# Kernel tuning notes

Hardware: AMD Instinct MI355X
Metric: run time of the kernel (lower is better)

## Reference

```python
import jax, jax.numpy as jnp
import numpy as np

DIM = 1024
NUM_HEADS = 16
MASKED = True


def setup_inputs() -> dict:
    key = jax.random.key(0)
    ks = jax.random.split(key, 9)
    B, S, D = 2, 2048, DIM
    return {
        "x": jax.random.normal(ks[0], (B, S, D), dtype=jnp.float32),
        "Wq": jax.random.normal(ks[1], (D, D), dtype=jnp.float32),
        "bq": jax.random.normal(ks[2], (D,), dtype=jnp.float32),
        "Wk": jax.random.normal(ks[3], (D, D), dtype=jnp.float32),
        "bk": jax.random.normal(ks[4], (D,), dtype=jnp.float32),
        "Wv": jax.random.normal(ks[5], (D, D), dtype=jnp.float32),
        "bv": jax.random.normal(ks[6], (D,), dtype=jnp.float32),
        "Wo": jax.random.normal(ks[7], (D, D), dtype=jnp.float32),
        "bo": jax.random.normal(ks[8], (D,), dtype=jnp.float32),
    }


def _mha(x, Wq, bq, Wk, bk, Wv, bv, Wo, bo):
    B, S, D = x.shape
    H = NUM_HEADS
    hd = D // H
    # projections (torch Linear stores [out,in]; here W is [out,in], x @ W.T + b)
    q = x @ Wq.T + bq
    k = x @ Wk.T + bk
    v = x @ Wv.T + bv
    # [B, H, S, hd]
    q = q.reshape(B, S, H, hd).transpose(0, 2, 1, 3)
    k = k.reshape(B, S, H, hd).transpose(0, 2, 1, 3)
    v = v.reshape(B, S, H, hd).transpose(0, 2, 1, 3)
    scores = jnp.einsum("bhqd,bhkd->bhqk", q, k) / jnp.sqrt(jnp.asarray(hd, x.dtype))
    if MASKED:
        mask = jnp.tril(jnp.ones((S, S), dtype=bool))
        scores = jnp.where(mask, scores, -jnp.inf)
    attn = jax.nn.softmax(scores, axis=-1)
    out = jnp.einsum("bhqk,bhkd->bhqd", attn, v)
    out = out.transpose(0, 2, 1, 3).reshape(B, S, D)
    return out @ Wo.T + bo


def reference(x, Wq, bq, Wk, bk, Wv, bv, Wo, bo):
    return _mha(x, Wq, bq, Wk, bk, Wv, bv, Wo, bo)
```

## Files before the change

kernel.cpp:

```cpp
#include <hip/hip_runtime.h>

typedef unsigned short u16;
typedef unsigned int u32;
typedef __attribute__((ext_vector_type(4))) float f32x4;
typedef __attribute__((ext_vector_type(8))) __bf16 bf16x8;

#define L2E 1.4426950408889634f

__device__ __forceinline__ u16 f2bf(float f) { return __builtin_bit_cast(u16, (__bf16)f); }
__device__ __forceinline__ float bf2f(u16 h) { return (float)__builtin_bit_cast(__bf16, h); }
__device__ __forceinline__ f32x4 mfma16(bf16x8 a, bf16x8 b, f32x4 c) {
  return __builtin_amdgcn_mfma_f32_16x16x32_bf16(a, b, c, 0, 0, 0);
}
__device__ __forceinline__ void gl_lds16(const u16* g, u16* l) {
  __builtin_amdgcn_global_load_lds((__attribute__((address_space(1))) void*)g,
                                   (__attribute__((address_space(3))) void*)l,
                                   16, 0, 0);
}
__device__ __forceinline__ f32x4 fzero() {
  f32x4 v = {0.f, 0.f, 0.f, 0.f};
  return v;
}

__global__ void k_prep(const float* __restrict__ x, const float* __restrict__ Wq,
                       const float* __restrict__ Wk, const float* __restrict__ Wv,
                       const float* __restrict__ Wo,
                       u16* __restrict__ xh, u16* __restrict__ xl,
                       u16* __restrict__ wqh, u16* __restrict__ wql,
                       u16* __restrict__ wkh, u16* __restrict__ wkl,
                       u16* __restrict__ wvb, u16* __restrict__ wob) {
  int i = (blockIdx.x * 256 + threadIdx.x) * 4;
  const float* src;
  u16* hi;
  u16* lo;
  int j;
  if (i < 4194304)      { src = x;  hi = xh;  lo = xl;      j = i; }
  else if (i < 5242880) { src = Wq; hi = wqh; lo = wql;     j = i - 4194304; }
  else if (i < 6291456) { src = Wk; hi = wkh; lo = wkl;     j = i - 5242880; }
  else if (i < 7340032) { src = Wv; hi = wvb; lo = nullptr; j = i - 6291456; }
  else                  { src = Wo; hi = wob; lo = nullptr; j = i - 7340032; }
  float4 v = *(const float4*)(src + j);
  float vv[4] = {v.x, v.y, v.z, v.w};
  u16 hh[4];
#pragma unroll
  for (int t = 0; t < 4; ++t) hh[t] = f2bf(vv[t]);
  *(ushort4*)(hi + j) = make_ushort4(hh[0], hh[1], hh[2], hh[3]);
  if (lo) {
    u16 ll[4];
#pragma unroll
    for (int t = 0; t < 4; ++t) ll[t] = f2bf(vv[t] - bf2f(hh[t]));
    *(ushort4*)(lo + j) = make_ushort4(ll[0], ll[1], ll[2], ll[3]);
  }
}

template <int SPLIT, int EPI>
__device__ __forceinline__ void gemm_body(
    u16* sm, const u16* __restrict__ Ah, const u16* __restrict__ Al,
    const u16* __restrict__ Bh, const u16* __restrict__ Bl,
    const float* __restrict__ bias, float scale,
    u16* __restrict__ oH, u16* __restrict__ oL, float* __restrict__ oF,
    int m0, int n0) {
  u16* sAh = sm;
  u16* sBh = sm + 8192;
  u16* sAl = SPLIT ? (sm + 16384) : sm;
  u16* sBl = SPLIT ? (sm + 24576) : sm;

  const int tid = threadIdx.x;
  const int lane = tid & 63, w = tid >> 6;
  const int wm = w >> 1, wn = w & 1;
  const int fr = lane & 15, fg = lane >> 4;
  const int strow = tid >> 3;
  const int stcb = (tid & 7) * 16;

  f32x4 acc[4][4];
#pragma unroll
  for (int i = 0; i < 4; ++i)
#pragma unroll
    for (int j = 0; j < 4; ++j) acc[i][j] = fzero();

  for (int kk = 0; kk < 1024; kk += 64) {
    __syncthreads();
#pragma unroll
    for (int c = 0; c < 4; ++c) {
      int row = c * 32 + strow;
      int srcc = (stcb ^ (((row >> 2) & 1) << 5)) >> 1;
      int dstc = row * 64 + (stcb >> 1);
      gl_lds16(Ah + (size_t)(m0 + row) * 1024 + kk + srcc, sAh + dstc);
      gl_lds16(Bh + (size_t)(n0 + row) * 1024 + kk + srcc, sBh + dstc);
      if constexpr (SPLIT) {
        gl_lds16(Al + (size_t)(m0 + row) * 1024 + kk + srcc, sAl + dstc);
        gl_lds16(Bl + (size_t)(n0 + row) * 1024 + kk + srcc, sBl + dstc);
      }
    }
    __syncthreads();

#pragma unroll
    for (int kk2 = 0; kk2 < 2; ++kk2) {
      bf16x8 ah[4], bh[4], al[4], bl[4];
#pragma unroll
      for (int i = 0; i < 4; ++i) {
        int ra = wm * 64 + i * 16 + fr;
        int ca = (kk2 * 64 + fg * 16) ^ (((ra >> 2) & 1) << 5);
        ah[i] = *(const bf16x8*)(sAh + ra * 64 + (ca >> 1));
        if constexpr (SPLIT) al[i] = *(const bf16x8*)(sAl + ra * 64 + (ca >> 1));
        int rb = wn * 64 + i * 16 + fr;
        int cb = (kk2 * 64 + fg * 16) ^ (((rb >> 2) & 1) << 5);
        bh[i] = *(const bf16x8*)(sBh + rb * 64 + (cb >> 1));
        if constexpr (SPLIT) bl[i] = *(const bf16x8*)(sBl + rb * 64 + (cb >> 1));
      }
      __builtin_amdgcn_s_setprio(1);
#pragma unroll
      for (int i = 0; i < 4; ++i)
#pragma unroll
        for (int j = 0; j < 4; ++j) {
          acc[i][j] = mfma16(ah[i], bh[j], acc[i][j]);
          if constexpr (SPLIT) {
            acc[i][j] = mfma16(ah[i], bl[j], acc[i][j]);
            acc[i][j] = mfma16(al[i], bh[j], acc[i][j]);
          }
        }
      __builtin_amdgcn_s_setprio(0);
    }
  }

#pragma unroll
  for (int i = 0; i < 4; ++i)
#pragma unroll
    for (int j = 0; j < 4; ++j) {
      int cg = n0 + wn * 64 + j * 16 + fr;
      float bv = bias[cg];
      if constexpr (EPI == 1) {
        int rgb = m0 + wm * 64 + i * 16 + fg * 4;
        int b = rgb >> 11, s = rgb & 2047, hd2 = cg >> 6, dd = cg & 63;
        u16 hv[4];
#pragma unroll
        for (int r = 0; r < 4; ++r) hv[r] = f2bf((acc[i][j][r] + bv) * scale);
        *(ushort4*)(oH + ((size_t)((b * 16 + hd2) * 64 + dd)) * 2048 + s) =
            make_ushort4(hv[0], hv[1], hv[2], hv[3]);
      } else {
#pragma unroll
        for (int r = 0; r < 4; ++r) {
          int rg = m0 + wm * 64 + i * 16 + fg * 4 + r;
          float val = (acc[i][j][r] + bv) * scale;
          if constexpr (EPI == 0) {
            int b = rg >> 11, s = rg & 2047, hd2 = cg >> 6, dd = cg & 63;
            size_t off = ((size_t)((b * 16 + hd2) * 2048 + s)) * 64 + dd;
            u16 hv = f2bf(val);
            oH[off] = hv;
            oL[off] = f2bf(val - bf2f(hv));
          } else {
            oF[(size_t)rg * 1024 + cg] = val;
          }
        }
      }
    }
}

__global__ __launch_bounds__(256, 2) void k_qkv(
    const u16* __restrict__ xh, const u16* __restrict__ xl,
    const u16* __restrict__ wqh, const u16* __restrict__ wql,
    const u16* __restrict__ wkh, const u16* __restrict__ wkl,
    const u16* __restrict__ wvb,
    const float* __restrict__ bq, const float* __restrict__ bk,
    const float* __restrict__ bv,
    u16* __restrict__ qh, u16* __restrict__ ql,
    u16* __restrict__ kh, u16* __restrict__ kl, u16* __restrict__ vt) {
  __shared__ u16 sm[32768];
  const int d = blockIdx.x;
  const int xcd = d & 7, j = d >> 3;
  const int m0 = (xcd * 4 + (j & 3)) * 128;
  const int pn = j >> 2;
  const int proj = pn >> 3, n0 = (pn & 7) * 128;
  if (proj == 0)
    gemm_body<1, 0>(sm, xh, xl, wqh, wql, bq, 0.125f * L2E, qh, ql, nullptr, m0, n0);
  else if (proj == 1)
    gemm_body<1, 0>(sm, xh, xl, wkh, wkl, bk, 1.0f, kh, kl, nullptr, m0, n0);
  else
    gemm_body<0, 1>(sm, xh, nullptr, wvb, nullptr, bv, 1.0f, vt, nullptr, nullptr, m0, n0);
}

__global__ __launch_bounds__(256, 4) void k_oproj(
    const u16* __restrict__ A, const u16* __restrict__ B,
    const float* __restrict__ bias, float* __restrict__ out) {
  __shared__ u16 sm[12288];
  u16* sA = sm;
  u16* sB = sm + 4096;

  const int tid = threadIdx.x;
  const int lane = tid & 63, w = tid >> 6;
  const int fr = lane & 15, fg = lane >> 4;
  const int m0 = blockIdx.x * 64, n0 = blockIdx.y * 128;
  const int strow = tid >> 3;
  const int stcb = (tid & 7) * 16;

  f32x4 acc[4][2];
#pragma unroll
  for (int i = 0; i < 4; ++i)
#pragma unroll
    for (int jj = 0; jj < 2; ++jj) acc[i][jj] = fzero();

  for (int kk = 0; kk < 1024; kk += 64) {
    __syncthreads();
#pragma unroll
    for (int c = 0; c < 2; ++c) {
      int row = c * 32 + strow;
      int srcc = (stcb ^ (((row >> 2) & 1) << 5)) >> 1;
      gl_lds16(A + (size_t)(m0 + row) * 1024 + kk + srcc, sA + row * 64 + (stcb >> 1));
    }
#pragma unroll
    for (int c = 0; c < 4; ++c) {
      int row = c * 32 + strow;
      int srcc = (stcb ^ (((row >> 2) & 1) << 5)) >> 1;
      gl_lds16(B + (size_t)(n0 + row) * 1024 + kk + srcc, sB + row * 64 + (stcb >> 1));
    }
    __syncthreads();

#pragma unroll
    for (int kk2 = 0; kk2 < 2; ++kk2) {
      bf16x8 af[4], bf_[2];
#pragma unroll
      for (int i = 0; i < 4; ++i) {
        int ra = i * 16 + fr;
        int ca = (kk2 * 64 + fg * 16) ^ (((ra >> 2) & 1) << 5);
        af[i] = *(const bf16x8*)(sA + ra * 64 + (ca >> 1));
      }
#pragma unroll
      for (int jj = 0; jj < 2; ++jj) {
        int rb = w * 32 + jj * 16 + fr;
        int cb = (kk2 * 64 + fg * 16) ^ (((rb >> 2) & 1) << 5);
        bf_[jj] = *(const bf16x8*)(sB + rb * 64 + (cb >> 1));
      }
      __builtin_amdgcn_s_setprio(1);
#pragma unroll
      for (int i = 0; i < 4; ++i)
#pragma unroll
        for (int jj = 0; jj < 2; ++jj) acc[i][jj] = mfma16(af[i], bf_[jj], acc[i][jj]);
      __builtin_amdgcn_s_setprio(0);
    }
  }

#pragma unroll
  for (int i = 0; i < 4; ++i)
#pragma unroll
    for (int jj = 0; jj < 2; ++jj) {
      int cg = n0 + w * 32 + jj * 16 + fr;
      float bv = bias[cg];
#pragma unroll
      for (int r = 0; r < 4; ++r) {
        int rg = m0 + i * 16 + fg * 4 + r;
        out[(size_t)rg * 1024 + cg] = acc[i][jj][r] + bv;
      }
    }
}

__global__ __launch_bounds__(256, 2) void k_attn(
    const u16* __restrict__ Qh, const u16* __restrict__ Ql,
    const u16* __restrict__ Kh, const u16* __restrict__ Kl,
    const u16* __restrict__ Vt, u16* __restrict__ Oa) {
  __shared__ u16 sKh[3][4096], sKl[3][4096], sVt[3][4096];

  const int tid = threadIdx.x;
  const int lane = tid & 63, w = tid >> 6;
  const int fr = lane & 15, fg = lane >> 4;

  const int d = blockIdx.x;
  const int g = d >> 3;
  const int bh = (d & 7) * 4 + (g & 3);
  const int pr = g >> 2;

  const size_t base = (size_t)bh * 131072;
  const u16* Qh_p = Qh + base;
  const u16* Ql_p = Ql + base;
  const u16* Kh_p = Kh + base;
  const u16* Kl_p = Kl + base;
  const u16* Vt_p = Vt + base;
  const int bb = bh >> 4, hh = bh & 15;

  const int srow = tid >> 3, scb8 = tid & 7;

  auto STAGE = [&](int t, int c) {
#pragma unroll
    for (int r2 = 0; r2 < 2; ++r2) {
      int prow = r2 * 32 + srow;
      int kvs = (prow & 32) | ((prow & 16) >> 2) | ((prow & 12) << 1) | (prow & 3);
      int cbk = scb8 ^ (prow & 7);
      gl_lds16(Kh_p + ((size_t)(t * 64 + kvs)) * 64 + cbk * 8, &sKh[c][prow * 64 + scb8 * 8]);
      gl_lds16(Kl_p + ((size_t)(t * 64 + kvs)) * 64 + cbk * 8, &sKl[c][prow * 64 + scb8 * 8]);
      gl_lds16(Vt_p + (size_t)prow * 2048 + t * 64 + cbk * 8, &sVt[c][prow * 64 + scb8 * 8]);
    }
  };

  for (int half = 0; half < 2; ++half) {
    const int j = half ? (31 - pr) : pr;
    const int nt = j + 1;
    const int qrow = j * 64 + w * 16 + fr;

    if (half) asm volatile("s_barrier" ::: "memory");
    int cur = 0;
    STAGE(0, 0);

    bf16x8 qhf[2], qlf[2];
#pragma unroll
    for (int ks = 0; ks < 2; ++ks) {
      qhf[ks] = *(const bf16x8*)(Qh_p + (size_t)qrow * 64 + ks * 32 + fg * 8);
      qlf[ks] = *(const bf16x8*)(Ql_p + (size_t)qrow * 64 + ks * 32 + fg * 8);
    }

    float mx = -1e30f, l = 0.f;
    f32x4 o[4];
#pragma unroll
    for (int f = 0; f < 4; ++f) o[f] = fzero();

    for (int t = 0; t < nt; ++t) {
      int nxt = cur + 1;
      if (nxt == 3) nxt = 0;
      if (t + 1 < nt) {
        STAGE(t + 1, nxt);
        asm volatile("s_waitcnt vmcnt(6)" ::: "memory");
      } else {
        asm volatile("s_waitcnt vmcnt(0)" ::: "memory");
      }
      asm volatile("s_barrier" ::: "memory");

      const u16* kbh = sKh[cur];
      const u16* kbl = sKl[cur];
      const u16* vbb = sVt[cur];

      f32x4 sc[4];
      __builtin_amdgcn_s_setprio(1);
#pragma unroll
      for (int f = 0; f < 4; ++f) {
        f32x4 a = fzero();
#pragma unroll
        for (int ks = 0; ks < 2; ++ks) {
          int row = f * 16 + fr;
          int cb = (fg + 4 * ks) ^ (fr & 7);
          bf16x8 khv = *(const bf16x8*)(kbh + row * 64 + cb * 8);
          bf16x8 klv = *(const bf16x8*)(kbl + row * 64 + cb * 8);
          a = mfma16(khv, qhf[ks], a);
          a = mfma16(khv, qlf[ks], a);
          a = mfma16(klv, qhf[ks], a);
        }
        sc[f] = a;
      }
      __builtin_amdgcn_s_setprio(0);

      if (t == nt - 1) {
#pragma unroll
        for (int f = 0; f < 4; ++f) {
          int kvb = t * 64 + (f >> 1) * 32 + fg * 8 + (f & 1) * 4;
#pragma unroll
          for (int r = 0; r < 4; ++r)
            if (kvb + r > qrow) sc[f][r] = -1e30f;
        }
      }

      float pm = -1e30f;
#pragma unroll
      for (int f = 0; f < 4; ++f)
#pragma unroll
        for (int r = 0; r < 4; ++r) pm = fmaxf(pm, sc[f][r]);
      pm = fmaxf(pm, __shfl_xor(pm, 16, 64));
      pm = fmaxf(pm, __shfl_xor(pm, 32, 64));

      const bool resc = __any(pm > mx + 11.5f);
      float alp = 1.0f;
      if (resc) {
        float mn = fmaxf(mx, pm);
        alp = exp2f(mx - mn);
        mx = mn;
      }

      float pp[4][4];
      float ps = 0.f;
#pragma unroll
      for (int f = 0; f < 4; ++f) {
#pragma unroll
        for (int r = 0; r < 4; ++r) {
          pp[f][r] = exp2f(sc[f][r] - mx);
          ps += pp[f][r];
        }
      }
      ps += __shfl_xor(ps, 16, 64);
      ps += __shfl_xor(ps, 32, 64);
      l = l * alp + ps;

      if (resc) {
        float alpb[4];
#pragma unroll
        for (int r = 0; r < 4; ++r) alpb[r] = __shfl(alp, fg * 4 + r, 64);
#pragma unroll
        for (int f = 0; f < 4; ++f)
#pragma unroll
          for (int r = 0; r < 4; ++r) o[f][r] *= alpb[r];
      }

      __builtin_amdgcn_s_setprio(1);
#pragma unroll
      for (int ks = 0; ks < 2; ++ks) {
        bf16x8 pa;
#pragma unroll
        for (int jj = 0; jj < 4; ++jj) {
          pa[jj] = (__bf16)pp[2 * ks][jj];
          pa[4 + jj] = (__bf16)pp[2 * ks + 1][jj];
        }
#pragma unroll
        for (int f = 0; f < 4; ++f) {
          int row = f * 16 + fr;
          int cb = (fg + 4 * ks) ^ (fr & 7);
          bf16x8 vb = *(const bf16x8*)(vbb + row * 64 + cb * 8);
          o[f] = mfma16(pa, vb, o[f]);
        }
      }
      __builtin_amdgcn_s_setprio(0);

      cur = nxt;
    }

    float lb[4];
#pragma unroll
    for (int r = 0; r < 4; ++r) lb[r] = __shfl(l, fg * 4 + r, 64);
#pragma unroll
    for (int f = 0; f < 4; ++f)
#pragma unroll
      for (int r = 0; r < 4; ++r) {
        int qg = j * 64 + w * 16 + fg * 4 + r;
        float val = o[f][r] / lb[r];
        Oa[((size_t)(bb * 2048 + qg)) * 1024 + hh * 64 + f * 16 + fr] = f2bf(val);
      }
  }
}

extern "C" void kernel_launch(void* const* d_in, const int* in_sizes, int n_in,
                              void* d_out, int out_size, void* d_ws, size_t ws_size,
                              hipStream_t stream) {
  const float* x  = (const float*)d_in[0];
  const float* Wq = (const float*)d_in[1];
  const float* bq = (const float*)d_in[2];
  const float* Wk = (const float*)d_in[3];
  const float* bk = (const float*)d_in[4];
  const float* Wv = (const float*)d_in[5];
  const float* bv = (const float*)d_in[6];
  const float* Wo = (const float*)d_in[7];
  const float* bo = (const float*)d_in[8];
  float* out = (float*)d_out;

  u16* ws  = (u16*)d_ws;
  u16* xh  = ws;
  u16* xl  = xh + 4194304;
  u16* wqh = xl + 4194304;
  u16* wql = wqh + 1048576;
  u16* wkh = wql + 1048576;
  u16* wkl = wkh + 1048576;
  u16* wvb = wkl + 1048576;
  u16* wob = wvb + 1048576;
  u16* qh  = wob + 1048576;
  u16* ql  = qh + 4194304;
  u16* kh  = ql + 4194304;
  u16* kl  = kh + 4194304;
  u16* vt  = kl + 4194304;
  u16* ao  = xh;

  k_prep<<<8192, 256, 0, stream>>>(x, Wq, Wk, Wv, Wo, xh, xl, wqh, wql, wkh, wkl, wvb, wob);
  k_qkv<<<768, 256, 0, stream>>>(xh, xl, wqh, wql, wkh, wkl, wvb, bq, bk, bv,
                                 qh, ql, kh, kl, vt);
  k_attn<<<512, 256, 0, stream>>>(qh, ql, kh, kl, vt, ao);
  k_oproj<<<dim3(64, 8), 256, 0, stream>>>(ao, wob, bo, out);
}
```

Baseline: 152.0 us.

## Split attention into one q-tile per block and load V directly to registers

```diff
diff --git a/kernel.cpp b/kernel.cpp
--- a/kernel.cpp
+++ b/kernel.cpp
@@ -253,20 +253,20 @@
     }
 }
 
-__global__ __launch_bounds__(256, 2) void k_attn(
+__global__ __launch_bounds__(256, 4) void k_attn(
     const u16* __restrict__ Qh, const u16* __restrict__ Ql,
     const u16* __restrict__ Kh, const u16* __restrict__ Kl,
     const u16* __restrict__ Vt, u16* __restrict__ Oa) {
-  __shared__ u16 sKh[3][4096], sKl[3][4096], sVt[3][4096];
+  __shared__ u16 sKh[2][4096], sKl[2][4096];
 
   const int tid = threadIdx.x;
   const int lane = tid & 63, w = tid >> 6;
   const int fr = lane & 15, fg = lane >> 4;
 
   const int d = blockIdx.x;
-  const int g = d >> 3;
-  const int bh = (d & 7) * 4 + (g & 3);
-  const int pr = g >> 2;
+  const int bh = (d & 7) * 4 + ((d >> 3) & 3);
+  const int j = 31 - (d >> 5);
+  const int nt = j + 1;
 
   const size_t base = (size_t)bh * 131072;
   const u16* Qh_p = Qh + base;
@@ -286,149 +286,144 @@
       int cbk = scb8 ^ (prow & 7);
       gl_lds16(Kh_p + ((size_t)(t * 64 + kvs)) * 64 + cbk * 8, &sKh[c][prow * 64 + scb8 * 8]);
       gl_lds16(Kl_p + ((size_t)(t * 64 + kvs)) * 64 + cbk * 8, &sKl[c][prow * 64 + scb8 * 8]);
-      gl_lds16(Vt_p + (size_t)prow * 2048 + t * 64 + cbk * 8, &sVt[c][prow * 64 + scb8 * 8]);
     }
   };
 
-  for (int half = 0; half < 2; ++half) {
-    const int j = half ? (31 - pr) : pr;
-    const int nt = j + 1;
-    const int qrow = j * 64 + w * 16 + fr;
-
-    if (half) asm volatile("s_barrier" ::: "memory");
-    int cur = 0;
-    STAGE(0, 0);
-
-    bf16x8 qhf[2], qlf[2];
+  const int qrow = j * 64 + w * 16 + fr;
+
+  STAGE(0, 0);
+
+  bf16x8 qhf[2], qlf[2];
+#pragma unroll
+  for (int ks = 0; ks < 2; ++ks) {
+    qhf[ks] = *(const bf16x8*)(Qh_p + (size_t)qrow * 64 + ks * 32 + fg * 8);
+    qlf[ks] = *(const bf16x8*)(Ql_p + (size_t)qrow * 64 + ks * 32 + fg * 8);
+  }
+
+  float mx = -1e30f, l = 0.f;
+  f32x4 o[4];
+#pragma unroll
+  for (int f = 0; f < 4; ++f) o[f] = fzero();
+
+  for (int t = 0; t < nt; ++t) {
+    const int cur = t & 1;
+
+    bf16x8 vf[2][4];
+#pragma unroll
+    for (int ks = 0; ks < 2; ++ks)
+#pragma unroll
+      for (int f = 0; f < 4; ++f)
+        vf[ks][f] = *(const bf16x8*)(Vt_p + (size_t)(f * 16 + fr) * 2048 + t * 64 +
+                                     ks * 32 + fg * 8);
+
+    if (t + 1 < nt) {
+      STAGE(t + 1, cur ^ 1);
+      asm volatile("s_waitcnt vmcnt(12)" ::: "memory");
+    } else {
+      asm volatile("s_waitcnt vmcnt(8)" ::: "memory");
+    }
+    asm volatile("s_barrier" ::: "memory");
+
+    const u16* kbh = sKh[cur];
+    const u16* kbl = sKl[cur];
+
+    f32x4 sc[4];
+    __builtin_amdgcn_s_setprio(1);
+#pragma unroll
+    for (int f = 0; f < 4; ++f) {
+      f32x4 a = fzero();
+#pragma unroll
+      for (int ks = 0; ks < 2; ++ks) {
+        int row = f * 16 + fr;
+        int cb = (fg + 4 * ks) ^ (fr & 7);
+        bf16x8 khv = *(const bf16x8*)(kbh + row * 64 + cb * 8);
+        bf16x8 klv = *(const bf16x8*)(kbl + row * 64 + cb * 8);
+        a = mfma16(khv, qhf[ks], a);
+        a = mfma16(khv, qlf[ks], a);
+        a = mfma16(klv, qhf[ks], a);
+      }
+      sc[f] = a;
+    }
+    __builtin_amdgcn_s_setprio(0);
+
+    if (t == nt - 1) {
+#pragma unroll
+      for (int f = 0; f < 4; ++f) {
+        int kvb = t * 64 + (f >> 1) * 32 + fg * 8 + (f & 1) * 4;
+#pragma unroll
+        for (int r = 0; r < 4; ++r)
+          if (kvb + r > qrow) sc[f][r] = -1e30f;
+      }
+    }
+
+    float pm = -1e30f;
+#pragma unroll
+    for (int f = 0; f < 4; ++f)
+#pragma unroll
+      for (int r = 0; r < 4; ++r) pm = fmaxf(pm, sc[f][r]);
+    pm = fmaxf(pm, __shfl_xor(pm, 16, 64));
+    pm = fmaxf(pm, __shfl_xor(pm, 32, 64));
+
+    const bool resc = __any(pm > mx + 11.5f);
+    float alp = 1.0f;
+    if (resc) {
+      float mn = fmaxf(mx, pm);
+      alp = exp2f(mx - mn);
+      mx = mn;
+    }
+
+    float pp[4][4];
+    float ps = 0.f;
+#pragma unroll
+    for (int f = 0; f < 4; ++f) {
+#pragma unroll
+      for (int r = 0; r < 4; ++r) {
+        pp[f][r] = exp2f(sc[f][r] - mx);
+        ps += pp[f][r];
+      }
+    }
+    ps += __shfl_xor(ps, 16, 64);
+    ps += __shfl_xor(ps, 32, 64);
+    l = l * alp + ps;
+
+    if (resc) {
+      float alpb[4];
+#pragma unroll
+      for (int r = 0; r < 4; ++r) alpb[r] = __shfl(alp, fg * 4 + r, 64);
+#pragma unroll
+      for (int f = 0; f < 4; ++f)
+#pragma unroll
+        for (int r = 0; r < 4; ++r) o[f][r] *= alpb[r];
+    }
+
+    __builtin_amdgcn_s_setprio(1);
 #pragma unroll
     for (int ks = 0; ks < 2; ++ks) {
-      qhf[ks] = *(const bf16x8*)(Qh_p + (size_t)qrow * 64 + ks * 32 + fg * 8);
-      qlf[ks] = *(const bf16x8*)(Ql_p + (size_t)qrow * 64 + ks * 32 + fg * 8);
-    }
-
-    float mx = -1e30f, l = 0.f;
-    f32x4 o[4];
-#pragma unroll
-    for (int f = 0; f < 4; ++f) o[f] = fzero();
-
-    for (int t = 0; t < nt; ++t) {
-      int nxt = cur + 1;
-      if (nxt == 3) nxt = 0;
-      if (t + 1 < nt) {
-        STAGE(t + 1, nxt);
-        asm volatile("s_waitcnt vmcnt(6)" ::: "memory");
-      } else {
-        asm volatile("s_waitcnt vmcnt(0)" ::: "memory");
-      }
-      asm volatile("s_barrier" ::: "memory");
-
-      const u16* kbh = sKh[cur];
-      const u16* kbl = sKl[cur];
-      const u16* vbb = sVt[cur];
-
-      f32x4 sc[4];
-      __builtin_amdgcn_s_setprio(1);
-#pragma unroll
-      for (int f = 0; f < 4; ++f) {
-        f32x4 a = fzero();
-#pragma unroll
-        for (int ks = 0; ks < 2; ++ks) {
-          int row = f * 16 + fr;
-          int cb = (fg + 4 * ks) ^ (fr & 7);
-          bf16x8 khv = *(const bf16x8*)(kbh + row * 64 + cb * 8);
-          bf16x8 klv = *(const bf16x8*)(kbl + row * 64 + cb * 8);
-          a = mfma16(khv, qhf[ks], a);
-          a = mfma16(khv, qlf[ks], a);
-          a = mfma16(klv, qhf[ks], a);
-        }
-        sc[f] = a;
-      }
-      __builtin_amdgcn_s_setprio(0);
-
-      if (t == nt - 1) {
-#pragma unroll
-        for (int f = 0; f < 4; ++f) {
-          int kvb = t * 64 + (f >> 1) * 32 + fg * 8 + (f & 1) * 4;
-#pragma unroll
-          for (int r = 0; r < 4; ++r)
-            if (kvb + r > qrow) sc[f][r] = -1e30f;
-        }
-      }
-
-      float pm = -1e30f;
-#pragma unroll
-      for (int f = 0; f < 4; ++f)
-#pragma unroll
-        for (int r = 0; r < 4; ++r) pm = fmaxf(pm, sc[f][r]);
-      pm = fmaxf(pm, __shfl_xor(pm, 16, 64));
-      pm = fmaxf(pm, __shfl_xor(pm, 32, 64));
-
-      const bool resc = __any(pm > mx + 11.5f);
-      float alp = 1.0f;
-      if (resc) {
-        float mn = fmaxf(mx, pm);
-        alp = exp2f(mx - mn);
-        mx = mn;
-      }
-
-      float pp[4][4];
-      float ps = 0.f;
-#pragma unroll
-      for (int f = 0; f < 4; ++f) {
-#pragma unroll
-        for (int r = 0; r < 4; ++r) {
-          pp[f][r] = exp2f(sc[f][r] - mx);
-          ps += pp[f][r];
-        }
-      }
-      ps += __shfl_xor(ps, 16, 64);
-      ps += __shfl_xor(ps, 32, 64);
-      l = l * alp + ps;
-
-      if (resc) {
-        float alpb[4];
-#pragma unroll
-        for (int r = 0; r < 4; ++r) alpb[r] = __shfl(alp, fg * 4 + r, 64);
-#pragma unroll
-        for (int f = 0; f < 4; ++f)
-#pragma unroll
-          for (int r = 0; r < 4; ++r) o[f][r] *= alpb[r];
-      }
-
-      __builtin_amdgcn_s_setprio(1);
-#pragma unroll
-      for (int ks = 0; ks < 2; ++ks) {
-        bf16x8 pa;
-#pragma unroll
-        for (int jj = 0; jj < 4; ++jj) {
-          pa[jj] = (__bf16)pp[2 * ks][jj];
-          pa[4 + jj] = (__bf16)pp[2 * ks + 1][jj];
-        }
-#pragma unroll
-        for (int f = 0; f < 4; ++f) {
-          int row = f * 16 + fr;
-          int cb = (fg + 4 * ks) ^ (fr & 7);
-          bf16x8 vb = *(const bf16x8*)(vbb + row * 64 + cb * 8);
-          o[f] = mfma16(pa, vb, o[f]);
-        }
-      }
-      __builtin_amdgcn_s_setprio(0);
-
-      cur = nxt;
-    }
-
-    float lb[4];
-#pragma unroll
-    for (int r = 0; r < 4; ++r) lb[r] = __shfl(l, fg * 4 + r, 64);
-#pragma unroll
-    for (int f = 0; f < 4; ++f)
-#pragma unroll
-      for (int r = 0; r < 4; ++r) {
-        int qg = j * 64 + w * 16 + fg * 4 + r;
-        float val = o[f][r] / lb[r];
-        Oa[((size_t)(bb * 2048 + qg)) * 1024 + hh * 64 + f * 16 + fr] = f2bf(val);
-      }
+      bf16x8 pa;
+#pragma unroll
+      for (int jj = 0; jj < 4; ++jj) {
+        pa[jj] = (__bf16)pp[2 * ks][jj];
+        pa[4 + jj] = (__bf16)pp[2 * ks + 1][jj];
+      }
+#pragma unroll
+      for (int f = 0; f < 4; ++f) o[f] = mfma16(pa, vf[ks][f], o[f]);
+    }
+    __builtin_amdgcn_s_setprio(0);
+
+    asm volatile("s_barrier" ::: "memory");
   }
+
+  float lb[4];
+#pragma unroll
+  for (int r = 0; r < 4; ++r) lb[r] = __shfl(l, fg * 4 + r, 64);
+#pragma unroll
+  for (int f = 0; f < 4; ++f)
+#pragma unroll
+    for (int r = 0; r < 4; ++r) {
+      int qg = j * 64 + w * 16 + fg * 4 + r;
+      float val = o[f][r] / lb[r];
+      Oa[((size_t)(bb * 2048 + qg)) * 1024 + hh * 64 + f * 16 + fr] = f2bf(val);
+    }
 }
 
 extern "C" void kernel_launch(void* const* d_in, const int* in_sizes, int n_in,
@@ -464,6 +459,6 @@
   k_prep<<<8192, 256, 0, stream>>>(x, Wq, Wk, Wv, Wo, xh, xl, wqh, wql, wkh, wkl, wvb, wob);
   k_qkv<<<768, 256, 0, stream>>>(xh, xl, wqh, wql, wkh, wkl, wvb, bq, bk, bv,
                                  qh, ql, kh, kl, vt);
-  k_attn<<<512, 256, 0, stream>>>(qh, ql, kh, kl, vt, ao);
+  k_attn<<<1024, 256, 0, stream>>>(qh, ql, kh, kl, vt, ao);
   k_oproj<<<dim3(64, 8), 256, 0, stream>>>(ao, wob, bo, out);
 }
```

Result: slower. 187.7 us (+23.5%).
